# Kernel optimization log

Hardware: AMD Instinct MI355X
Metric: run time of the kernel (lower is better)

Reference implementation:

```python
import jax, jax.numpy as jnp
import numpy as np

B = 2048       # batch
F_IN = 1024    # input feature dim
R_EMB = 1024   # rows of EmbedLinear sparse weight (new features)
NNZ_E = 65536  # nnz of embed sparse weight
F_OUT = 1024   # output dim of ExpandingLinear
NNZ_W = 131072 # nnz of main sparse weight [F_OUT, F_IN + R_EMB]
NNZ_B = 512    # nnz of sparse bias
F_MID = F_IN + R_EMB


def setup_inputs() -> dict:
    key = jax.random.key(0)
    ks = jax.random.split(key, 9)
    return {
        "x": jax.random.normal(ks[0], (B, F_IN), jnp.float32),
        "embed_rows": jax.random.randint(ks[1], (NNZ_E,), 0, R_EMB, jnp.int32),
        "embed_cols": jax.random.randint(ks[2], (NNZ_E,), 0, F_IN, jnp.int32),
        "embed_vals": jax.random.normal(ks[3], (NNZ_E,), jnp.float32) * 0.05,
        "w_rows": jax.random.randint(ks[4], (NNZ_W,), 0, F_OUT, jnp.int32),
        "w_cols": jax.random.randint(ks[5], (NNZ_W,), 0, F_MID, jnp.int32),
        "w_vals": jax.random.normal(ks[6], (NNZ_W,), jnp.float32) * 0.05,
        "bias_idx": jax.random.randint(ks[7], (NNZ_B,), 0, F_OUT, jnp.int32),
        "bias_vals": jax.random.normal(ks[8], (NNZ_B,), jnp.float32),
    }


def _spmm(rows, cols, vals, x, n_rows):
    # sparse COO [n_rows, F] @ x.T -> transposed: returns [B, n_rows]
    # (matches torch.sparse.mm(sparse_w, input.t()).t())
    g = vals[:, None] * x.T[cols]                              # [nnz, B] gather + scale
    return jax.ops.segment_sum(g, rows, num_segments=n_rows).T # scatter-add over rows


def reference(x, embed_rows, embed_cols, embed_vals,
              w_rows, w_cols, w_vals, bias_idx, bias_vals):
    # EmbedLinear.forward: sparse mm + ReLU + concat along features
    h = jax.nn.relu(_spmm(embed_rows, embed_cols, embed_vals, x, R_EMB))  # [B, R_EMB]
    x2 = jnp.concatenate([x, h], axis=1)                                   # [B, F_MID]
    # ExpandingLinear tail: sparse weight mm + densified sparse bias
    bias = jnp.zeros((F_OUT,), x.dtype).at[bias_idx].add(bias_vals)
    return _spmm(w_rows, w_cols, w_vals, x2, F_OUT) + bias[None, :]        # [B, F_OUT]
```

## Files before the change

### kernel.cpp

```cpp
#include <hip/hip_runtime.h>
#include <hip/hip_bf16.h>

#define B_SZ   2048
#define F_IN   1024
#define R_EMB  1024
#define F_OUT  1024
#define F_MID  2048
#define NNZ_E  65536
#define NNZ_W  131072
#define NNZ_B  512

typedef __bf16 bf16x8 __attribute__((ext_vector_type(8)));
typedef float  f32x16 __attribute__((ext_vector_type(16)));

__device__ inline void gload16(const void* g, void* l) {
    __builtin_amdgcn_global_load_lds(
        (const __attribute__((address_space(1))) void*)g,
        (__attribute__((address_space(3))) void*)l, 16, 0, 0);
}

__device__ inline ushort f2bf(float v) {
    __hip_bfloat16 h = __float2bfloat16(v);
    return *reinterpret_cast<ushort*>(&h);
}

__device__ inline float bf2f(ushort u) {
    uint w = (uint)u << 16;
    float f;
    __builtin_memcpy(&f, &w, 4);
    return f;
}

__device__ inline void bf16_scatter_add(ushort* addr, float val) {
    uint* word = (uint*)((uintptr_t)addr & ~(uintptr_t)3);
    const bool hi = ((uintptr_t)addr & 2) != 0;
    uint old = __hip_atomic_load(word, __ATOMIC_RELAXED, __HIP_MEMORY_SCOPE_AGENT);
    while (true) {
        ushort cur = hi ? (ushort)(old >> 16) : (ushort)(old & 0xffffu);
        ushort nv  = f2bf(bf2f(cur) + val);
        uint neww  = hi ? ((old & 0x0000ffffu) | ((uint)nv << 16))
                        : ((old & 0xffff0000u) | (uint)nv);
        uint prev = atomicCAS(word, old, neww);
        if (prev == old) break;
        old = prev;
    }
}

__global__ void k_zero4(float4* __restrict__ p, int n) {
    int i = blockIdx.x * blockDim.x + threadIdx.x;
    if (i < n) p[i] = make_float4(0.f, 0.f, 0.f, 0.f);
}

__global__ void k_prep(const float4* __restrict__ x, ushort* __restrict__ x2,
                       const int* __restrict__ er, const int* __restrict__ ec,
                       const float* __restrict__ ev,
                       const int* __restrict__ wr_, const int* __restrict__ wc_,
                       const float* __restrict__ wv,
                       const int* __restrict__ bi, const float* __restrict__ bv,
                       ushort* __restrict__ Ebf, ushort* __restrict__ Wbf,
                       float* __restrict__ biasd) {
    int b = blockIdx.x, t = threadIdx.x;
    if (b < 2048) {
        int i = b * 256 + t;
        int row = i >> 8, c4 = i & 255;
        float4 v = x[i];
        ((ushort4*)x2)[(size_t)row * (F_MID / 4) + c4] =
            make_ushort4(f2bf(v.x), f2bf(v.y), f2bf(v.z), f2bf(v.w));
    } else if (b < 2048 + NNZ_E / 256) {
        int i = (b - 2048) * 256 + t;
        bf16_scatter_add(&Ebf[(size_t)er[i] * F_IN + ec[i]], ev[i]);
    } else if (b < 2048 + NNZ_E / 256 + NNZ_W / 256) {
        int i = (b - 2048 - NNZ_E / 256) * 256 + t;
        bf16_scatter_add(&Wbf[(size_t)wr_[i] * F_MID + wc_[i]], wv[i]);
    } else {
        int i = (b - 2048 - NNZ_E / 256 - NNZ_W / 256) * 256 + t;
        if (i < NNZ_B) atomicAdd(&biasd[bi[i]], bv[i]);
    }
}

__global__ __launch_bounds__(256)
void k_gemmA(const ushort* __restrict__ x2,
             const ushort* __restrict__ Ebf,
             const ushort* __restrict__ Wbf,
             const float* __restrict__ biasd,
             float* __restrict__ out,
             ushort* __restrict__ hOut)
{
    constexpr int BK = 64, NT = 16;
    __shared__ ushort lds[2][3][64 * 64];
    const int tid = threadIdx.x;
    const int w = tid >> 6, l = tid & 63;
    const int wr = w >> 1, wc = w & 1;
    const int hi = l >> 5;

    const int blk = blockIdx.x;
    const int sw  = (blk & 7) * 64 + (blk >> 3);
    const int m0  = (sw >> 4) * 64;
    const int n0  = (sw & 15) * 64;

    const int arow = wr * 32 + (l & 31);
    const int brow = wc * 32 + (l & 31);
    const int xa = arow & 7, xb = brow & 7;

    const int srow = w * 8 + (l >> 3);
    const int ldst = w * 512 + l * 8;

    f32x16 accE = {}, accW = {};

    #define STAGE(buf, k0)                                                      \
        _Pragma("unroll")                                                       \
        for (int i = 0; i < 2; ++i) {                                           \
            int row = i * 32 + srow;                                            \
            int scol = (k0) + ((((l & 7) ^ (row & 7))) << 3);                   \
            gload16(x2  + (size_t)(m0 + row) * F_MID + scol,                    \
                    &lds[buf][0][i * 2048 + ldst]);                             \
            gload16(Ebf + (size_t)(n0 + row) * F_IN + scol,                     \
                    &lds[buf][1][i * 2048 + ldst]);                             \
            gload16(Wbf + (size_t)(n0 + row) * F_MID + scol,                    \
                    &lds[buf][2][i * 2048 + ldst]);                             \
        }

    STAGE(0, 0);
    __syncthreads();

    for (int t = 0; t < NT; ++t) {
        const int cur = t & 1;
        if (t + 1 < NT) STAGE(cur ^ 1, (t + 1) * BK);

        const ushort* sA  = &lds[cur][0][0];
        const ushort* sBE = &lds[cur][1][0];
        const ushort* sBW = &lds[cur][2][0];
        #pragma unroll
        for (int s = 0; s < 4; ++s) {
            const int c = s * 2 + hi;
            bf16x8 af = *(const bf16x8*)(sA  + arow * BK + ((c ^ xa) << 3));
            bf16x8 be = *(const bf16x8*)(sBE + brow * BK + ((c ^ xb) << 3));
            bf16x8 bw = *(const bf16x8*)(sBW + brow * BK + ((c ^ xb) << 3));
            accE = __builtin_amdgcn_mfma_f32_32x32x16_bf16(af, be, accE, 0, 0, 0);
            accW = __builtin_amdgcn_mfma_f32_32x32x16_bf16(af, bw, accW, 0, 0, 0);
        }
        __syncthreads();
    }
    #undef STAGE

    const int col = n0 + wc * 32 + (l & 31);
    const int r0  = m0 + wr * 32 + 4 * hi;
    const float bv = biasd[col];
    #pragma unroll
    for (int r = 0; r < 16; ++r) {
        const int row = r0 + (r & 3) + 8 * (r >> 2);
        hOut[(size_t)row * F_MID + col] = f2bf(fmaxf(accE[r], 0.f));
        out[(size_t)row * F_OUT + col]  = accW[r] + bv;
    }
}

__global__ __launch_bounds__(256)
void k_gemmB(const ushort* __restrict__ x2,
             const ushort* __restrict__ Wbf,
             float* __restrict__ out)
{
    constexpr int BK = 64, NT = 16;
    __shared__ ushort lds[2][2][64 * 64];
    const int tid = threadIdx.x;
    const int w = tid >> 6, l = tid & 63;
    const int wr = w >> 1, wc = w & 1;
    const int hi = l >> 5;

    const int blk = blockIdx.x;
    const int sw  = (blk & 7) * 64 + (blk >> 3);
    const int m0  = (sw >> 4) * 64;
    const int n0  = (sw & 15) * 64;

    const ushort* A  = x2 + F_IN;
    const ushort* Bm = Wbf + F_IN;

    const int arow = wr * 32 + (l & 31);
    const int brow = wc * 32 + (l & 31);
    const int xa = arow & 7, xb = brow & 7;

    const int srow = w * 8 + (l >> 3);
    const int ldst = w * 512 + l * 8;

    f32x16 acc = {};

    #define STAGE(buf, k0)                                                      \
        _Pragma("unroll")                                                       \
        for (int i = 0; i < 2; ++i) {                                           \
            int row = i * 32 + srow;                                            \
            int scol = (k0) + ((((l & 7) ^ (row & 7))) << 3);                   \
            gload16(A  + (size_t)(m0 + row) * F_MID + scol,                     \
                    &lds[buf][0][i * 2048 + ldst]);                             \
            gload16(Bm + (size_t)(n0 + row) * F_MID + scol,                     \
                    &lds[buf][1][i * 2048 + ldst]);                             \
        }

    STAGE(0, 0);
    __syncthreads();

    for (int t = 0; t < NT; ++t) {
        const int cur = t & 1;
        if (t + 1 < NT) STAGE(cur ^ 1, (t + 1) * BK);

        const ushort* sA = &lds[cur][0][0];
        const ushort* sB = &lds[cur][1][0];
        #pragma unroll
        for (int s = 0; s < 4; ++s) {
            const int c = s * 2 + hi;
            bf16x8 af = *(const bf16x8*)(sA + arow * BK + ((c ^ xa) << 3));
            bf16x8 bg = *(const bf16x8*)(sB + brow * BK + ((c ^ xb) << 3));
            acc = __builtin_amdgcn_mfma_f32_32x32x16_bf16(af, bg, acc, 0, 0, 0);
        }
        __syncthreads();
    }
    #undef STAGE

    const int col = n0 + wc * 32 + (l & 31);
    const int r0  = m0 + wr * 32 + 4 * hi;
    #pragma unroll
    for (int r = 0; r < 16; ++r) {
        const int row = r0 + (r & 3) + 8 * (r >> 2);
        out[(size_t)row * F_OUT + col] += acc[r];
    }
}

extern "C" void kernel_launch(void* const* d_in, const int* in_sizes, int n_in,
                              void* d_out, int out_size, void* d_ws, size_t ws_size,
                              hipStream_t stream) {
    const float* x          = (const float*)d_in[0];
    const int*   embed_rows = (const int*)  d_in[1];
    const int*   embed_cols = (const int*)  d_in[2];
    const float* embed_vals = (const float*)d_in[3];
    const int*   w_rows     = (const int*)  d_in[4];
    const int*   w_cols     = (const int*)  d_in[5];
    const float* w_vals     = (const float*)d_in[6];
    const int*   bias_idx   = (const int*)  d_in[7];
    const float* bias_vals  = (const float*)d_in[8];
    float* out = (float*)d_out;

    char* ws = (char*)d_ws;
    ushort* x2    = (ushort*)ws;
    float*  biasd = (float*)(ws + (20u << 20));
    ushort* Ebf   = (ushort*)(ws + (20u << 20) + 4096);
    ushort* Wbf   = (ushort*)(ws + (22u << 20) + 4096);

    k_zero4<<<1537, 256, 0, stream>>>((float4*)biasd, 393472);

    k_prep<<<2048 + NNZ_E / 256 + NNZ_W / 256 + NNZ_B / 256, 256, 0, stream>>>(
        (const float4*)x, x2,
        embed_rows, embed_cols, embed_vals,
        w_rows, w_cols, w_vals,
        bias_idx, bias_vals, Ebf, Wbf, biasd);

    k_gemmA<<<512, 256, 0, stream>>>(x2, Ebf, Wbf, biasd, out, x2 + F_IN);

    k_gemmB<<<512, 256, 0, stream>>>(x2, Wbf, out);
}
```

Measured before the change: 51.07 us.

## Merge x conversion into zeroing kernel and double gemmB K-tile depth

```diff
diff --git a/kernel.cpp b/kernel.cpp
--- a/kernel.cpp
+++ b/kernel.cpp
@@ -46,34 +46,37 @@
     }
 }
 
-__global__ void k_zero4(float4* __restrict__ p, int n) {
-    int i = blockIdx.x * blockDim.x + threadIdx.x;
-    if (i < n) p[i] = make_float4(0.f, 0.f, 0.f, 0.f);
-}
-
-__global__ void k_prep(const float4* __restrict__ x, ushort* __restrict__ x2,
-                       const int* __restrict__ er, const int* __restrict__ ec,
-                       const float* __restrict__ ev,
-                       const int* __restrict__ wr_, const int* __restrict__ wc_,
-                       const float* __restrict__ wv,
-                       const int* __restrict__ bi, const float* __restrict__ bv,
-                       ushort* __restrict__ Ebf, ushort* __restrict__ Wbf,
-                       float* __restrict__ biasd) {
+__global__ void k_zerocvt(float4* __restrict__ zbase,
+                          const float4* __restrict__ x, ushort* __restrict__ x2) {
     int b = blockIdx.x, t = threadIdx.x;
-    if (b < 2048) {
+    if (b < 1537) {
         int i = b * 256 + t;
+        if (i < 393472) zbase[i] = make_float4(0.f, 0.f, 0.f, 0.f);
+    } else {
+        int i = (b - 1537) * 256 + t;
         int row = i >> 8, c4 = i & 255;
         float4 v = x[i];
         ((ushort4*)x2)[(size_t)row * (F_MID / 4) + c4] =
             make_ushort4(f2bf(v.x), f2bf(v.y), f2bf(v.z), f2bf(v.w));
-    } else if (b < 2048 + NNZ_E / 256) {
-        int i = (b - 2048) * 256 + t;
+    }
+}
+
+__global__ void k_scatter(const int* __restrict__ er, const int* __restrict__ ec,
+                          const float* __restrict__ ev,
+                          const int* __restrict__ wr_, const int* __restrict__ wc_,
+                          const float* __restrict__ wv,
+                          const int* __restrict__ bi, const float* __restrict__ bv,
+                          ushort* __restrict__ Ebf, ushort* __restrict__ Wbf,
+                          float* __restrict__ biasd) {
+    int b = blockIdx.x, t = threadIdx.x;
+    if (b < NNZ_E / 256) {
+        int i = b * 256 + t;
         bf16_scatter_add(&Ebf[(size_t)er[i] * F_IN + ec[i]], ev[i]);
-    } else if (b < 2048 + NNZ_E / 256 + NNZ_W / 256) {
-        int i = (b - 2048 - NNZ_E / 256) * 256 + t;
+    } else if (b < NNZ_E / 256 + NNZ_W / 256) {
+        int i = (b - NNZ_E / 256) * 256 + t;
         bf16_scatter_add(&Wbf[(size_t)wr_[i] * F_MID + wc_[i]], wv[i]);
     } else {
-        int i = (b - 2048 - NNZ_E / 256 - NNZ_W / 256) * 256 + t;
+        int i = (b - NNZ_E / 256 - NNZ_W / 256) * 256 + t;
         if (i < NNZ_B) atomicAdd(&biasd[bi[i]], bv[i]);
     }
 }
@@ -159,8 +162,8 @@
              const ushort* __restrict__ Wbf,
              float* __restrict__ out)
 {
-    constexpr int BK = 64, NT = 16;
-    __shared__ ushort lds[2][2][64 * 64];
+    constexpr int BK = 128, NT = 8;
+    __shared__ ushort lds[2][2][64 * BK];
     const int tid = threadIdx.x;
     const int w = tid >> 6, l = tid & 63;
     const int wr = w >> 1, wc = w & 1;
@@ -178,20 +181,19 @@
     const int brow = wc * 32 + (l & 31);
     const int xa = arow & 7, xb = brow & 7;
 
-    const int srow = w * 8 + (l >> 3);
-    const int ldst = w * 512 + l * 8;
+    const int srow = tid >> 4, sslot = tid & 15;
 
     f32x16 acc = {};
 
     #define STAGE(buf, k0)                                                      \
         _Pragma("unroll")                                                       \
-        for (int i = 0; i < 2; ++i) {                                           \
-            int row = i * 32 + srow;                                            \
-            int scol = (k0) + ((((l & 7) ^ (row & 7))) << 3);                   \
+        for (int i = 0; i < 4; ++i) {                                           \
+            int row = i * 16 + srow;                                            \
+            int scol = (k0) + (((sslot ^ (row & 7))) << 3);                     \
             gload16(A  + (size_t)(m0 + row) * F_MID + scol,                     \
-                    &lds[buf][0][i * 2048 + ldst]);                             \
+                    &lds[buf][0][i * 2048 + tid * 8]);                          \
             gload16(Bm + (size_t)(n0 + row) * F_MID + scol,                     \
-                    &lds[buf][1][i * 2048 + ldst]);                             \
+                    &lds[buf][1][i * 2048 + tid * 8]);                          \
         }
 
     STAGE(0, 0);
@@ -204,7 +206,7 @@
         const ushort* sA = &lds[cur][0][0];
         const ushort* sB = &lds[cur][1][0];
         #pragma unroll
-        for (int s = 0; s < 4; ++s) {
+        for (int s = 0; s < 8; ++s) {
             const int c = s * 2 + hi;
             bf16x8 af = *(const bf16x8*)(sA + arow * BK + ((c ^ xa) << 3));
             bf16x8 bg = *(const bf16x8*)(sB + brow * BK + ((c ^ xb) << 3));
@@ -243,10 +245,10 @@
     ushort* Ebf   = (ushort*)(ws + (20u << 20) + 4096);
     ushort* Wbf   = (ushort*)(ws + (22u << 20) + 4096);
 
-    k_zero4<<<1537, 256, 0, stream>>>((float4*)biasd, 393472);
-
-    k_prep<<<2048 + NNZ_E / 256 + NNZ_W / 256 + NNZ_B / 256, 256, 0, stream>>>(
-        (const float4*)x, x2,
+    k_zerocvt<<<1537 + 2048, 256, 0, stream>>>((float4*)biasd,
+                                               (const float4*)x, x2);
+
+    k_scatter<<<NNZ_E / 256 + NNZ_W / 256 + (NNZ_B + 255) / 256, 256, 0, stream>>>(
         embed_rows, embed_cols, embed_vals,
         w_rows, w_cols, w_vals,
         bias_idx, bias_vals, Ebf, Wbf, biasd);
```

Measured after the change: 59.21 us. 15.9% more time.
